# Kernel optimization log

Measured on AMD Instinct MI355X. Metric: run time of the kernel, lower is better.

## Reference

```python
import jax, jax.numpy as jnp
import numpy as np

N, E = 20000, 320000
IN_DIM = OUT_DIM = E_IN = E_OUT = 128
BN_EPS = 1e-5

def _lrelu(x):
    return jnp.where(x >= 0, x, 0.1 * x)

def setup_inputs() -> dict:
    key = jax.random.key(0)
    ks = jax.random.split(key, 12)
    def w(k, shape):
        return jax.random.normal(k, shape, jnp.float32) * (shape[0] ** -0.5)
    return {
        "h": jax.random.normal(ks[0], (N, IN_DIM), jnp.float32),
        "edge_w": jax.random.normal(ks[1], (E, E_IN), jnp.float32),
        "W_node": w(ks[2], (IN_DIM, OUT_DIM)),
        "W_eedge": w(ks[3], (E_IN, E_IN)),
        "W_esf": w(ks[4], (E_IN, 1)),
        "W_fuse": w(ks[5], (2 * OUT_DIM + E_IN, OUT_DIM)),
        "b_fuse": jnp.zeros((OUT_DIM,), jnp.float32),
        "W_attn": w(ks[6], (OUT_DIM, 1)),
        "W_conc": w(ks[7], (2 * OUT_DIM + E_IN, OUT_DIM)),
        "b_conc": jnp.zeros((OUT_DIM,), jnp.float32),
        "bn_gamma": jnp.ones((E_IN,), jnp.float32),
        "bn_beta": jnp.zeros((E_IN,), jnp.float32),
        "W_aggre": w(ks[8], (2 * OUT_DIM + 2 * E_IN, E_OUT)),
        "src": jax.random.randint(ks[9], (E,), 0, N),
        "dst": jax.random.randint(ks[10], (E,), 0, N),
    }

def reference(h, edge_w, W_node, W_eedge, W_esf, W_fuse, b_fuse, W_attn,
              W_conc, b_conc, bn_gamma, bn_beta, W_aggre, src, dst):
    # eval mode: dropout = identity, BatchNorm uses running stats (mean 0, var 1)
    hn = h @ W_node                       # embed_node -> ndata['h'] = ndata['oh']
    # self_attention: ow = embed_edge(w); w = edge_sf_atten(lrelu(ow)) * ow
    ow = edge_w @ W_eedge                 # [E, e_in]
    w1 = (_lrelu(ow) @ W_esf) * ow        # [E, e_in]
    # inter_attention
    hs, hd = hn[src], hn[dst]             # [E, out]
    sat = jnp.concatenate([hs, hd, w1], axis=-1)          # [E, 2*out+e_in]
    inw = _lrelu(sat @ W_fuse + b_fuse)                   # [E, out]
    a = inw @ W_attn                                      # [E, 1]
    w2 = a * w1                                           # edata['w']
    # reduce_func2: segment softmax over incoming edges (grouped by dst)
    s = a[:, 0]
    m = jax.ops.segment_max(s, dst, num_segments=N)
    e = jnp.exp(s - m[dst])
    denom = jax.ops.segment_sum(e, dst, num_segments=N)
    alpha = (e / denom[dst])[:, None]                     # [E, 1]
    t = jnp.concatenate([hs, w2], axis=-1)                # [E, out+e_in]
    h_agg = jax.ops.segment_sum(alpha * t, dst, num_segments=N)  # [N, out+e_in]
    h_new = jnp.concatenate([h_agg, hn], axis=-1) @ W_conc + b_conc
    # DGL only updates nodes that received messages; zero-indegree keep embed_node(h)
    indeg = jax.ops.segment_sum(jnp.ones((E,), jnp.float32), dst, num_segments=N)
    h_out = jnp.where(indeg[:, None] > 0, h_new, hn)      # [N, out]
    # edge_calc: BN(w2) then aggre_embed_edge(cat(src_h, dst_h, bn_w, ow))
    w_bn = (w2 / jnp.sqrt(jnp.float32(1.0) + BN_EPS)) * bn_gamma + bn_beta
    z = jnp.concatenate([h_out[src], h_out[dst], w_bn, ow], axis=-1)
    w_out = z @ W_aggre                                   # [E, e_out]
    return h_out, w_out, sat
```

## Files before the change

kernel.cpp:

```cpp
#include <hip/hip_runtime.h>
#include <hip/hip_bf16.h>

#define TB 256
#define TBM 512
#define BM 64
#define BK 32
#define BN 128
#define ASTR 68
#define MAXD 160

static constexpr int NN = 20000;
static constexpr int NE = 320000;

static constexpr long long OFF_HN   = 0;
static constexpr long long OFF_OW   = 2560000;
static constexpr long long OFF_S    = 43520000;
static constexpr long long OFF_DEN  = 43840000;
static constexpr long long OFF_CUR  = 43860000;
static constexpr long long OFF_HAGG = 43880000;
static constexpr long long OFF_WT   = 49000000;
static constexpr long long WS_FLOATS = 49140000;

static constexpr int U_E = 0;
static constexpr int U_F = 32768;
static constexpr int U_A = 131072;

static constexpr long long OUT_HOUT = 0;
static constexpr long long OUT_WOUT = 2560000;
static constexpr long long OUT_SAT  = 43520000;

typedef __attribute__((ext_vector_type(8))) short s8v;
typedef __attribute__((ext_vector_type(4))) float f32x4;
typedef __attribute__((ext_vector_type(8))) unsigned short u16x8;
typedef __attribute__((ext_vector_type(4))) unsigned short u16x4;

#define MFMA16(a,b,c) __builtin_amdgcn_mfma_f32_16x16x32_bf16(a,b,c,0,0,0)

__device__ __forceinline__ float lrelu(float x){ return x >= 0.f ? x : 0.1f*x; }

__device__ __forceinline__ void gl16(const void* g, void* l){
    __builtin_amdgcn_global_load_lds(
        (const __attribute__((address_space(1))) void*)g,
        (__attribute__((address_space(3))) void*)l, 16, 0, 0);
}

__device__ __forceinline__ void split1(float f, unsigned short& hi, unsigned short& lo){
    __hip_bfloat16 h = __float2bfloat16(f);
    float hf = __bfloat162float(h);
    __hip_bfloat16 l = __float2bfloat16(f - hf);
    hi = __builtin_bit_cast(unsigned short, h);
    lo = __builtin_bit_cast(unsigned short, l);
}
__device__ __forceinline__ void split8(float4 a, float4 b, s8v& hi, s8v& lo){
    float v[8] = {a.x,a.y,a.z,a.w,b.x,b.y,b.z,b.w};
#pragma unroll
    for (int j = 0; j < 8; ++j){
        unsigned short hs, ls;
        split1(v[j], hs, ls);
        hi[j] = (short)hs; lo[j] = (short)ls;
    }
}
__device__ __forceinline__ float bfpair(unsigned short h, unsigned short l){
    return __uint_as_float(((unsigned)h)<<16) + __uint_as_float(((unsigned)l)<<16);
}

__device__ __forceinline__ int lds_a(int row, int g){
    return row*32 + ((g ^ (row & 3)) << 3);
}

__device__ __forceinline__ void store_At(float (*Ast)[ASTR], int k4, int r, float4 v){
    Ast[k4+0][r] = v.x; Ast[k4+1][r] = v.y; Ast[k4+2][r] = v.z; Ast[k4+3][r] = v.w;
}
__device__ __forceinline__ void mm_chunk(const float (*Ast)[ASTR], const float (*Bs)[BN],
                                         int r0, int c0, float acc[4][8]){
#pragma unroll 4
    for (int k = 0; k < BK; ++k){
        const float4 av = *(const float4*)&Ast[k][r0];
        const float4 b0 = *(const float4*)&Bs[k][c0];
        const float4 b1 = *(const float4*)&Bs[k][64 + c0];
        const float a0=av.x, a1=av.y, a2=av.z, a3=av.w;
        const float b[8] = {b0.x,b0.y,b0.z,b0.w,b1.x,b1.y,b1.z,b1.w};
#pragma unroll
        for (int j = 0; j < 8; ++j){
            acc[0][j] = fmaf(a0, b[j], acc[0][j]);
            acc[1][j] = fmaf(a1, b[j], acc[1][j]);
            acc[2][j] = fmaf(a2, b[j], acc[2][j]);
            acc[3][j] = fmaf(a3, b[j], acc[3][j]);
        }
    }
}
__device__ __forceinline__ void load_B(const float* __restrict__ W, int kc,
                                       float (*Bs)[BN], int tid){
#pragma unroll
    for (int p = 0; p < 4; ++p){
        int idx = p*TB + tid;
        int row = idx >> 5;
        int c4  = (idx & 31) << 2;
        *(float4*)&Bs[row][c4] = *(const float4*)&W[(size_t)(kc+row)*BN + c4];
    }
}

__device__ __forceinline__ float blockMax(float v, float* sh4){
#pragma unroll
    for (int m = 32; m; m >>= 1) v = fmaxf(v, __shfl_xor(v, m));
    if ((threadIdx.x & 63) == 0) sh4[threadIdx.x >> 6] = v;
    __syncthreads();
    float r = fmaxf(fmaxf(sh4[0], sh4[1]), fmaxf(sh4[2], sh4[3]));
    __syncthreads();
    return r;
}
__device__ __forceinline__ float blockSum(float v, float* sh4){
#pragma unroll
    for (int m = 32; m; m >>= 1) v += __shfl_xor(v, m);
    if ((threadIdx.x & 63) == 0) sh4[threadIdx.x >> 6] = v;
    __syncthreads();
    float r = sh4[0] + sh4[1] + sh4[2] + sh4[3];
    __syncthreads();
    return r;
}

__global__ __launch_bounds__(TB) void k_prep(const float* __restrict__ We,
                                             const float* __restrict__ Wf,
                                             const float* __restrict__ Wa,
                                             unsigned short* __restrict__ wt,
                                             int* __restrict__ cur){
    int id = blockIdx.x*TB + threadIdx.x;
    if (id < NN) cur[id] = 0;
    unsigned short hs, ls;
    if (id < 16384){
        int n = id >> 7, k = id & 127;
        split1(We[(size_t)k*128 + n], hs, ls);
        wt[U_E + id] = hs; wt[U_E + 16384 + id] = ls;
    } else if (id < 65536){
        int local = id - 16384;
        int n = local / 384, k = local - n*384;
        split1(Wf[(size_t)k*128 + n], hs, ls);
        wt[U_F + local] = hs; wt[U_F + 49152 + local] = ls;
    } else if (id < 131072){
        int local = id - 65536;
        int n = local >> 9, k = local & 511;
        split1(Wa[(size_t)k*128 + n], hs, ls);
        wt[U_A + local] = hs; wt[U_A + 65536 + local] = ls;
    }
}

__global__ __launch_bounds__(TB) void kB_count(const int* __restrict__ dst,
                                               int* __restrict__ cur){
    int e = blockIdx.x*TB + threadIdx.x;
    atomicAdd(&cur[dst[e]], 1);
}
__global__ __launch_bounds__(TB) void kC_scan(int* __restrict__ cur,
                                              int* __restrict__ offs){
    __shared__ int part[TB];
    __shared__ int spre[TB];
    const int tid = threadIdx.x;
    const int CH = (NN + TB - 1) / TB;
    const int base = tid * CH;
    int sum = 0;
    for (int i = 0; i < CH; ++i){ int idx = base + i; if (idx < NN) sum += cur[idx]; }
    part[tid] = sum;
    __syncthreads();
    if (tid == 0){ int r = 0; for (int i = 0; i < TB; ++i){ spre[i] = r; r += part[i]; } }
    __syncthreads();
    int run = spre[tid];
    for (int i = 0; i < CH; ++i){
        int idx = base + i;
        if (idx < NN){ int c = cur[idx]; offs[idx] = run; cur[idx] = run; run += c; }
    }
}
__global__ __launch_bounds__(TB) void kD_scatter(const int* __restrict__ dst,
                                                 int* __restrict__ cur,
                                                 int* __restrict__ eidx){
    int e = blockIdx.x*TB + threadIdx.x;
    int p = atomicAdd(&cur[dst[e]], 1);
    eidx[p] = e;
}

__global__ __launch_bounds__(TB) void k1_hn(const float* __restrict__ h,
                                            const float* __restrict__ Wn,
                                            unsigned short* __restrict__ hnH,
                                            unsigned short* __restrict__ hnL){
    __shared__ float Ast[BK][ASTR];
    __shared__ float Bs[BK][BN];
    const int tid = threadIdx.x;
    const int rbase = blockIdx.x * BM;
    const int tc = tid & 15, tr = tid >> 4;
    const int r0 = tr*4, c0 = tc*4;
    float acc[4][8] = {};
    for (int kc = 0; kc < 128; kc += BK){
        __syncthreads();
        {
            int lr = tid >> 3, k4 = (tid & 7) << 2;
#pragma unroll
            for (int p = 0; p < 2; ++p){
                int r = p*32 + lr;
                int rr = rbase + r; if (rr >= NN) rr = NN-1;
                float4 v = *(const float4*)&h[(size_t)rr*128 + kc + k4];
                store_At(Ast, k4, r, v);
            }
        }
        load_B(Wn, kc, Bs, tid);
        __syncthreads();
        mm_chunk(Ast, Bs, r0, c0, acc);
    }
#pragma unroll
    for (int i = 0; i < 4; ++i){
        int rr = rbase + r0 + i;
        if (rr < NN){
            u16x4 h0, l0, h1, l1;
#pragma unroll
            for (int j = 0; j < 4; ++j){
                unsigned short hs, ls;
                split1(acc[i][j], hs, ls);   h0[j] = hs; l0[j] = ls;
                split1(acc[i][4+j], hs, ls); h1[j] = hs; l1[j] = ls;
            }
            *(u16x4*)&hnH[(size_t)rr*128 + c0] = h0;
            *(u16x4*)&hnL[(size_t)rr*128 + c0] = l0;
            *(u16x4*)&hnH[(size_t)rr*128 + 64 + c0] = h1;
            *(u16x4*)&hnL[(size_t)rr*128 + 64 + c0] = l1;
        }
    }
}


__global__ __launch_bounds__(TBM) void k2_mfma(const float* __restrict__ ew,
                                               const unsigned short* __restrict__ wtH,
                                               const unsigned short* __restrict__ wtL,
                                               const float* __restrict__ Wesf,
                                               unsigned short* __restrict__ owH,
                                               unsigned short* __restrict__ owL,
                                               float* __restrict__ sat){
    __shared__ __align__(16) unsigned short Ah[2][4096], Al[2][4096], Bh[2][4096], Bl[2][4096];
    __shared__ float sEsf[128];
    const int tid = threadIdx.x;
    const long long rbase = (long long)blockIdx.x * 128;
    const int lane = tid & 63, w = tid >> 6;
    const int ls = lane & 15, lg = lane >> 4;
    const int srow = tid >> 2, sg = tid & 3;
    const int gsw = sg ^ (srow & 3);
    const int aslot = srow*32 + (gsw << 3);
    if (tid < 128) sEsf[tid] = Wesf[tid];
    f32x4 acc[8] = {};
    auto stage = [&](int nb, int t){
        const int kc = t*32;
        gl16(&wtH[srow*128 + kc + gsw*8], &Bh[nb][w*512]);
        gl16(&wtL[srow*128 + kc + gsw*8], &Bl[nb][w*512]);
        const float* p = &ew[(rbase + srow)*128 + kc + sg*8];
        float4 v0 = *(const float4*)p, v1 = *(const float4*)(p+4);
        s8v hi, lo; split8(v0, v1, hi, lo);
        *(s8v*)&Ah[nb][aslot] = hi; *(s8v*)&Al[nb][aslot] = lo;
    };
    stage(0, 0);
    __syncthreads();
    int cur = 0;
    for (int t = 0; t < 4; ++t){
        if (t+1 < 4) stage(cur^1, t+1);
        s8v ah = *(const s8v*)&Ah[cur][lds_a(w*16 + ls, lg)];
        s8v al = *(const s8v*)&Al[cur][lds_a(w*16 + ls, lg)];
#pragma unroll
        for (int ct = 0; ct < 8; ++ct){
            int c = ct*16 + ls;
            s8v bh = *(const s8v*)&Bh[cur][lds_a(c,lg)];
            s8v bl = *(const s8v*)&Bl[cur][lds_a(c,lg)];
            acc[ct] = MFMA16(ah, bh, acc[ct]);
            acc[ct] = MFMA16(ah, bl, acc[ct]);
            acc[ct] = MFMA16(al, bh, acc[ct]);
        }
        __syncthreads();
        cur ^= 1;
    }
#pragma unroll
    for (int reg = 0; reg < 4; ++reg){
        float p = 0.f;
#pragma unroll
        for (int ct = 0; ct < 8; ++ct)
            p += lrelu(acc[ct][reg]) * sEsf[ct*16 + ls];
#pragma unroll
        for (int m = 1; m < 16; m <<= 1) p += __shfl_xor(p, m);
        long long orow = rbase + w*16 + lg*4 + reg;
#pragma unroll
        for (int ct = 0; ct < 8; ++ct){
            float o = acc[ct][reg];
            int col = ct*16 + ls;
            sat[orow*384 + 256 + col] = p * o;
            unsigned short hs_, ls_; split1(o, hs_, ls_);
            owH[orow*128 + col] = hs_;
            owL[orow*128 + col] = ls_;
        }
    }
}

__global__ __launch_bounds__(TBM) void k3_mfma(const unsigned short* __restrict__ hnH,
                                               const unsigned short* __restrict__ hnL,
                                               const unsigned short* __restrict__ wtH,
                                               const unsigned short* __restrict__ wtL,
                                               const float* __restrict__ bf,
                                               const float* __restrict__ Wattn,
                                               const int* __restrict__ src,
                                               const int* __restrict__ dst,
                                               float* __restrict__ sat,
                                               float* __restrict__ w2,
                                               float* __restrict__ s_ws){
    __shared__ __align__(16) unsigned short Ah[2][4096], Al[2][4096], Bh[2][4096], Bl[2][4096];
    __shared__ float sBf[128], sAtt[128];
    __shared__ int sSrc[128], sDst[128];
    const int tid = threadIdx.x;
    const long long rbase = (long long)blockIdx.x * 128;
    const int lane = tid & 63, w = tid >> 6;
    const int ls = lane & 15, lg = lane >> 4;
    const int srow = tid >> 2, sg = tid & 3;
    const int gsw = sg ^ (srow & 3);
    const int aslot = srow*32 + (gsw << 3);
    if (tid < 128){
        sBf[tid] = bf[tid]; sAtt[tid] = Wattn[tid];
        sSrc[tid] = src[rbase + tid]; sDst[tid] = dst[rbase + tid];
    }
    __syncthreads();
    f32x4 acc[8] = {};
    auto stage = [&](int nb, int t){
        const int kc = t*32;
        gl16(&wtH[srow*384 + kc + gsw*8], &Bh[nb][w*512]);
        gl16(&wtL[srow*384 + kc + gsw*8], &Bl[nb][w*512]);
        long long e = rbase + srow;
        if (kc < 256){
            int node = (kc < 128) ? sSrc[srow] : sDst[srow];
            int col0 = kc & 127;
            gl16(&hnH[(size_t)node*128 + col0 + gsw*8], &Ah[nb][w*512]);
            gl16(&hnL[(size_t)node*128 + col0 + gsw*8], &Al[nb][w*512]);
            u16x8 hv = *(const u16x8*)&hnH[(size_t)node*128 + col0 + sg*8];
            u16x8 lv = *(const u16x8*)&hnL[(size_t)node*128 + col0 + sg*8];
            float f[8];
#pragma unroll
            for (int j = 0; j < 8; ++j)
                f[j] = __uint_as_float(((unsigned)hv[j])<<16)
                     + __uint_as_float(((unsigned)lv[j])<<16);
            float4 v0 = {f[0],f[1],f[2],f[3]}, v1 = {f[4],f[5],f[6],f[7]};
            *(float4*)&sat[e*384 + kc + sg*8] = v0;
            *(float4*)&sat[e*384 + kc + sg*8 + 4] = v1;
        } else {
            const float* p = &sat[e*384 + kc + sg*8];
            float4 v0 = *(const float4*)p, v1 = *(const float4*)(p+4);
            s8v hi, lo; split8(v0, v1, hi, lo);
            *(s8v*)&Ah[nb][aslot] = hi; *(s8v*)&Al[nb][aslot] = lo;
        }
    };
    stage(0, 0);
    __syncthreads();
    int cur = 0;
    for (int t = 0; t < 12; ++t){
        if (t+1 < 12) stage(cur^1, t+1);
        s8v ah = *(const s8v*)&Ah[cur][lds_a(w*16 + ls, lg)];
        s8v al = *(const s8v*)&Al[cur][lds_a(w*16 + ls, lg)];
#pragma unroll
        for (int ct = 0; ct < 8; ++ct){
            int c = ct*16 + ls;
            s8v bh = *(const s8v*)&Bh[cur][lds_a(c,lg)];
            s8v bl = *(const s8v*)&Bl[cur][lds_a(c,lg)];
            acc[ct] = MFMA16(ah, bh, acc[ct]);
            acc[ct] = MFMA16(ah, bl, acc[ct]);
            acc[ct] = MFMA16(al, bh, acc[ct]);
        }
        __syncthreads();
        cur ^= 1;
    }
#pragma unroll
    for (int reg = 0; reg < 4; ++reg){
        float p = 0.f;
#pragma unroll
        for (int ct = 0; ct < 8; ++ct){
            int col = ct*16 + ls;
            p += lrelu(acc[ct][reg] + sBf[col]) * sAtt[col];
        }
#pragma unroll
        for (int m = 1; m < 16; m <<= 1) p += __shfl_xor(p, m);
        long long orow = rbase + w*16 + lg*4 + reg;
        if (ls == 0) s_ws[orow] = p;
#pragma unroll
        for (int ct = 0; ct < 8; ++ct){
            int col = ct*16 + ls;
            float w1v = sat[orow*384 + 256 + col];
            w2[orow*128 + col] = p * w1v;
        }
    }
}

__global__ __launch_bounds__(TB) void k5_agg(const float* __restrict__ s,
                                             const unsigned short* __restrict__ hnH,
                                             const unsigned short* __restrict__ hnL,
                                             const float* __restrict__ w2,
                                             const int* __restrict__ src,
                                             const int* __restrict__ eidx,
                                             const int* __restrict__ offs,
                                             const int* __restrict__ cur,
                                             float* __restrict__ hagg,
                                             float* __restrict__ den){
    __shared__ int   sE[MAXD];
    __shared__ int   sSrc[MAXD];
    __shared__ float sA[MAXD];
    __shared__ float sh4[4];
    const int n = blockIdx.x, tid = threadIdx.x;
    const int start = offs[n];
    const int deg = cur[n] - start;
    for (int i = tid; i < deg && i < MAXD; i += TB) sE[i] = eidx[start+i];
    __syncthreads();
    if (tid == 0 && deg > 1){
        int dd = deg < MAXD ? deg : MAXD;
        for (int i = 1; i < dd; ++i){
            int key = sE[i], j = i-1;
            while (j >= 0 && sE[j] > key){ sE[j+1] = sE[j]; --j; }
            sE[j+1] = key;
        }
    }
    __syncthreads();
    float lm = -3.402823466e38f;
    for (int i = tid; i < deg; i += TB){
        int e = (i < MAXD) ? sE[i] : eidx[start+i];
        lm = fmaxf(lm, s[e]);
    }
    const float m = blockMax(lm, sh4);
    float lsum = 0.f;
    for (int i = tid; i < deg; i += TB){
        int e = (i < MAXD) ? sE[i] : eidx[start+i];
        lsum += expf(s[e] - m);
    }
    const float denom = blockSum(lsum, sh4);
    for (int i = tid; i < deg && i < MAXD; i += TB){
        int e = sE[i];
        sA[i] = expf(s[e] - m) / denom;
        sSrc[i] = src[e];
    }
    __syncthreads();
    float acc = 0.f;
    const bool lo = tid < 128;
    for (int i = 0; i < deg; ++i){
        int e, sI; float a;
        if (i < MAXD){ e = sE[i]; a = sA[i]; sI = sSrc[i]; }
        else { e = eidx[start+i]; a = expf(s[e]-m)/denom; sI = src[e]; }
        float v = lo ? bfpair(hnH[(size_t)sI*128 + tid], hnL[(size_t)sI*128 + tid])
                     : w2[(size_t)e*128 + (tid-128)];
        acc = fmaf(a, v, acc);
    }
    hagg[(size_t)n*256 + tid] = acc;
    if (tid == 0) den[n] = (deg > 0) ? denom : 0.f;
}

__global__ __launch_bounds__(TB) void k6_conc(const float* hagg,
                                              const unsigned short* __restrict__ hnH,
                                              const unsigned short* __restrict__ hnL,
                                              const float* __restrict__ Wc,
                                              const float* __restrict__ bc,
                                              const float* __restrict__ den,
                                              float* __restrict__ hout,
                                              unsigned short* houtHL){
    __shared__ float Ast[BK][ASTR];
    __shared__ float Bs[BK][BN];
    __shared__ float sBc[BN];
    const int tid = threadIdx.x;
    const int rbase = blockIdx.x * BM;
    const int tc = tid & 15, tr = tid >> 4;
    const int r0 = tr*4, c0 = tc*4;
    if (tid < BN) sBc[tid] = bc[tid];
    float acc[4][8] = {};
    for (int chunk = 0; chunk < 12; ++chunk){
        int kc = chunk * BK;
        __syncthreads();
        {
            int lr = tid >> 3, k4 = (tid & 7) << 2;
#pragma unroll
            for (int p = 0; p < 2; ++p){
                int r = p*32 + lr;
                int rr = rbase + r; if (rr >= NN) rr = NN-1;
                float4 v;
                if (chunk < 8) v = *(const float4*)&hagg[(size_t)rr*256 + kc + k4];
                else {
                    int cb = (kc - 256) + k4;
                    u16x4 hh = *(const u16x4*)&hnH[(size_t)rr*128 + cb];
                    u16x4 ll = *(const u16x4*)&hnL[(size_t)rr*128 + cb];
                    v.x = bfpair(hh[0], ll[0]); v.y = bfpair(hh[1], ll[1]);
                    v.z = bfpair(hh[2], ll[2]); v.w = bfpair(hh[3], ll[3]);
                }
                store_At(Ast, k4, r, v);
            }
        }
        load_B(Wc, kc, Bs, tid);
        __syncthreads();
        mm_chunk(Ast, Bs, r0, c0, acc);
    }
#pragma unroll
    for (int i = 0; i < 4; ++i){
        int rr = rbase + r0 + i;
        if (rr >= NN) continue;
        bool keep = den[rr] > 0.f;
        float o[8];
#pragma unroll
        for (int j = 0; j < 8; ++j){
            int col = (j < 4) ? (c0 + j) : (60 + c0 + j);
            float fb = bfpair(hnH[(size_t)rr*128 + col], hnL[(size_t)rr*128 + col]);
            o[j] = keep ? acc[i][j] + sBc[col] : fb;
        }
        float4 o0 = {o[0],o[1],o[2],o[3]}, o1 = {o[4],o[5],o[6],o[7]};
        *(float4*)&hout[(size_t)rr*128 + c0] = o0;
        *(float4*)&hout[(size_t)rr*128 + 64 + c0] = o1;
        u16x4 h0, l0, h1, l1;
#pragma unroll
        for (int j = 0; j < 4; ++j){
            unsigned short hs, ls2;
            split1(o[j], hs, ls2);   h0[j] = hs; l0[j] = ls2;
            split1(o[4+j], hs, ls2); h1[j] = hs; l1[j] = ls2;
        }
        *(u16x4*)&houtHL[(size_t)rr*512 + c0] = h0;
        *(u16x4*)&houtHL[(size_t)rr*512 + 128 + c0] = l0;
        *(u16x4*)&houtHL[(size_t)rr*512 + 64 + c0] = h1;
        *(u16x4*)&houtHL[(size_t)rr*512 + 128 + 64 + c0] = l1;
    }
}

__global__ __launch_bounds__(TBM) void k7_mfma(const unsigned short* __restrict__ houtHL,
                                               const unsigned short* __restrict__ owH,
                                               const unsigned short* __restrict__ owL,
                                               const float* __restrict__ gamma,
                                               const float* __restrict__ beta,
                                               const unsigned short* __restrict__ wtH,
                                               const unsigned short* __restrict__ wtL,
                                               const int* __restrict__ src,
                                               const int* __restrict__ dst,
                                               float* __restrict__ w2out){
    __shared__ __align__(16) unsigned short Ah[2][4096], Al[2][4096], Bh[2][4096], Bl[2][4096];
    __shared__ float sGam[128], sBet[128];
    __shared__ int sSrc[128], sDst[128];
    const int tid = threadIdx.x;
    const long long rbase = (long long)blockIdx.x * 128;
    const int lane = tid & 63, w = tid >> 6;
    const int ls = lane & 15, lg = lane >> 4;
    const int srow = tid >> 2, sg = tid & 3;
    const int gsw = sg ^ (srow & 3);
    const int aslot = srow*32 + (gsw << 3);
    const float ISR = 0.9999950000374997f;
    if (tid < 128){
        sGam[tid] = gamma[tid] * ISR; sBet[tid] = beta[tid];
        sSrc[tid] = src[rbase + tid]; sDst[tid] = dst[rbase + tid];
    }
    __syncthreads();
    f32x4 acc[8] = {};
    auto stage = [&](int nb, int t){
        const int kc = t*32;
        gl16(&wtH[srow*512 + kc + gsw*8], &Bh[nb][w*512]);
        gl16(&wtL[srow*512 + kc + gsw*8], &Bl[nb][w*512]);
        long long e = rbase + srow;
        if (kc < 256){
            int node = (kc < 128) ? sSrc[srow] : sDst[srow];
            int col0 = kc & 127;
            gl16(&houtHL[(size_t)node*512 + col0 + gsw*8], &Ah[nb][w*512]);
            gl16(&houtHL[(size_t)node*512 + 128 + col0 + gsw*8], &Al[nb][w*512]);
        } else if (kc < 384){
            int cb = (kc - 256) + sg*8;
            const float* p = &w2out[e*128 + cb];
            float4 v0 = *(const float4*)p, v1 = *(const float4*)(p+4);
            v0.x = fmaf(v0.x, sGam[cb+0], sBet[cb+0]);
            v0.y = fmaf(v0.y, sGam[cb+1], sBet[cb+1]);
            v0.z = fmaf(v0.z, sGam[cb+2], sBet[cb+2]);
            v0.w = fmaf(v0.w, sGam[cb+3], sBet[cb+3]);
            v1.x = fmaf(v1.x, sGam[cb+4], sBet[cb+4]);
            v1.y = fmaf(v1.y, sGam[cb+5], sBet[cb+5]);
            v1.z = fmaf(v1.z, sGam[cb+6], sBet[cb+6]);
            v1.w = fmaf(v1.w, sGam[cb+7], sBet[cb+7]);
            s8v hi, lo; split8(v0, v1, hi, lo);
            *(s8v*)&Ah[nb][aslot] = hi; *(s8v*)&Al[nb][aslot] = lo;
        } else {
            int col0 = kc - 384;
            gl16(&owH[e*128 + col0 + gsw*8], &Ah[nb][w*512]);
            gl16(&owL[e*128 + col0 + gsw*8], &Al[nb][w*512]);
        }
    };
    stage(0, 0);
    __syncthreads();
    int cur = 0;
    for (int t = 0; t < 16; ++t){
        if (t+1 < 16) stage(cur^1, t+1);
        s8v ah = *(const s8v*)&Ah[cur][lds_a(w*16 + ls, lg)];
        s8v al = *(const s8v*)&Al[cur][lds_a(w*16 + ls, lg)];
#pragma unroll
        for (int ct = 0; ct < 8; ++ct){
            int c = ct*16 + ls;
            s8v bh = *(const s8v*)&Bh[cur][lds_a(c,lg)];
            s8v bl = *(const s8v*)&Bl[cur][lds_a(c,lg)];
            acc[ct] = MFMA16(ah, bh, acc[ct]);
            acc[ct] = MFMA16(ah, bl, acc[ct]);
            acc[ct] = MFMA16(al, bh, acc[ct]);
        }
        __syncthreads();
        cur ^= 1;
    }
#pragma unroll
    for (int reg = 0; reg < 4; ++reg){
        long long orow = rbase + w*16 + lg*4 + reg;
#pragma unroll
        for (int ct = 0; ct < 8; ++ct)
            w2out[orow*128 + ct*16 + ls] = acc[ct][reg];
    }
}

extern "C" void kernel_launch(void* const* d_in, const int* in_sizes, int n_in,
                              void* d_out, int out_size, void* d_ws, size_t ws_size,
                              hipStream_t stream){
    (void)in_sizes; (void)n_in; (void)out_size;
    const float* h       = (const float*)d_in[0];
    const float* edge_w  = (const float*)d_in[1];
    const float* W_node  = (const float*)d_in[2];
    const float* W_eedge = (const float*)d_in[3];
    const float* W_esf   = (const float*)d_in[4];
    const float* W_fuse  = (const float*)d_in[5];
    const float* b_fuse  = (const float*)d_in[6];
    const float* W_attn  = (const float*)d_in[7];
    const float* W_conc  = (const float*)d_in[8];
    const float* b_conc  = (const float*)d_in[9];
    const float* gamma   = (const float*)d_in[10];
    const float* beta    = (const float*)d_in[11];
    const float* W_aggre = (const float*)d_in[12];
    const int*   src     = (const int*)d_in[13];
    const int*   dst     = (const int*)d_in[14];

    float* out    = (float*)d_out;
    float* o_hout = out + OUT_HOUT;
    float* o_wout = out + OUT_WOUT;
    float* o_sat  = out + OUT_SAT;

    if (ws_size < (size_t)WS_FLOATS * 4) return;
    float* ws     = (float*)d_ws;
    unsigned short* w_hnH = (unsigned short*)(ws + OFF_HN);
    unsigned short* w_hnL = w_hnH + (size_t)NN*128;
    unsigned short* w_owH = (unsigned short*)(ws + OFF_OW);
    unsigned short* w_owL = w_owH + (size_t)NE*128;
    float* w_s    = ws + OFF_S;
    float* w_den  = ws + OFF_DEN;
    int*   w_cur  = (int*)(ws + OFF_CUR);
    float* w_hagg = ws + OFF_HAGG;
    unsigned short* w_houtHL = (unsigned short*)w_hagg;
    unsigned short* w_wt = (unsigned short*)(ws + OFF_WT);

    int* w_eidx = (int*)o_hout;
    int* w_offs = w_eidx + NE;

    hipLaunchKernelGGL(k_prep,    dim3(131072/TB), dim3(TB), 0, stream,
                       W_eedge, W_fuse, W_aggre, w_wt, w_cur);
    hipLaunchKernelGGL(kB_count,  dim3(NE/TB), dim3(TB), 0, stream, dst, w_cur);
    hipLaunchKernelGGL(kC_scan,   dim3(1), dim3(TB), 0, stream, w_cur, w_offs);
    hipLaunchKernelGGL(kD_scatter,dim3(NE/TB), dim3(TB), 0, stream, dst, w_cur, w_eidx);
    hipLaunchKernelGGL(k1_hn,     dim3((NN+BM-1)/BM), dim3(TB), 0, stream, h, W_node,
                       w_hnH, w_hnL);
    hipLaunchKernelGGL(k2_mfma,   dim3(NE/128), dim3(TBM), 0, stream, edge_w,
                       w_wt + U_E, w_wt + U_E + 128*128, W_esf,
                       w_owH, w_owL, o_sat);
    hipLaunchKernelGGL(k3_mfma,   dim3(NE/128), dim3(TBM), 0, stream, w_hnH, w_hnL,
                       w_wt + U_F, w_wt + U_F + 128*384, b_fuse, W_attn,
                       src, dst, o_sat, o_wout, w_s);
    hipLaunchKernelGGL(k5_agg,    dim3(NN), dim3(TB), 0, stream, w_s, w_hnH, w_hnL, o_wout,
                       src, w_eidx, w_offs, w_cur, w_hagg, w_den);
    hipLaunchKernelGGL(k6_conc,   dim3((NN+BM-1)/BM), dim3(TB), 0, stream, w_hagg,
                       w_hnH, w_hnL, W_conc, b_conc, w_den, o_hout, w_houtHL);
    hipLaunchKernelGGL(k7_mfma,   dim3(NE/128), dim3(TBM), 0, stream, w_houtHL,
                       w_owH, w_owL, gamma, beta,
                       w_wt + U_A, w_wt + U_A + 128*512,
                       src, dst, o_wout);
}
```

Before: 834.4 us.

## Pack hn hi/lo pairs, drop w2 materialization, use wave-per-node aggregation

k1_hn now also writes a packed array holding each bf16 hi/lo pair in one 32-bit word, kept in the w_out output buffer as scratch. k3, k5 and k6 read that packed array instead of two separate 16-bit arrays. k3 no longer writes the E×128 w2 tensor: k5 and k7 rebuild it from w1 (stored in sat) scaled by the per-edge attention score s. k5 runs one 64-lane wave per node, four nodes per block, and replaces the single-thread insertion sort and block-wide reductions with a parallel rank sort and wave shuffles. The aim is to cut global memory traffic and serialization, at the cost of an extra packed write in k1 and more strided reads of sat.

```diff
diff --git a/kernel.cpp b/kernel.cpp
--- a/kernel.cpp
+++ b/kernel.cpp
@@ -31,7 +31,6 @@
 
 typedef __attribute__((ext_vector_type(8))) short s8v;
 typedef __attribute__((ext_vector_type(4))) float f32x4;
-typedef __attribute__((ext_vector_type(8))) unsigned short u16x8;
 typedef __attribute__((ext_vector_type(4))) unsigned short u16x4;
 
 #define MFMA16(a,b,c) __builtin_amdgcn_mfma_f32_16x16x32_bf16(a,b,c,0,0,0)
@@ -60,8 +59,8 @@
         hi[j] = (short)hs; lo[j] = (short)ls;
     }
 }
-__device__ __forceinline__ float bfpair(unsigned short h, unsigned short l){
-    return __uint_as_float(((unsigned)h)<<16) + __uint_as_float(((unsigned)l)<<16);
+__device__ __forceinline__ float bfp(unsigned p){
+    return __uint_as_float(p & 0xffff0000u) + __uint_as_float(p << 16);
 }
 
 __device__ __forceinline__ int lds_a(int row, int g){
@@ -98,25 +97,6 @@
         int c4  = (idx & 31) << 2;
         *(float4*)&Bs[row][c4] = *(const float4*)&W[(size_t)(kc+row)*BN + c4];
     }
-}
-
-__device__ __forceinline__ float blockMax(float v, float* sh4){
-#pragma unroll
-    for (int m = 32; m; m >>= 1) v = fmaxf(v, __shfl_xor(v, m));
-    if ((threadIdx.x & 63) == 0) sh4[threadIdx.x >> 6] = v;
-    __syncthreads();
-    float r = fmaxf(fmaxf(sh4[0], sh4[1]), fmaxf(sh4[2], sh4[3]));
-    __syncthreads();
-    return r;
-}
-__device__ __forceinline__ float blockSum(float v, float* sh4){
-#pragma unroll
-    for (int m = 32; m; m >>= 1) v += __shfl_xor(v, m);
-    if ((threadIdx.x & 63) == 0) sh4[threadIdx.x >> 6] = v;
-    __syncthreads();
-    float r = sh4[0] + sh4[1] + sh4[2] + sh4[3];
-    __syncthreads();
-    return r;
 }
 
 __global__ __launch_bounds__(TB) void k_prep(const float* __restrict__ We,
@@ -179,7 +159,8 @@
 __global__ __launch_bounds__(TB) void k1_hn(const float* __restrict__ h,
                                             const float* __restrict__ Wn,
                                             unsigned short* __restrict__ hnH,
-                                            unsigned short* __restrict__ hnL){
+                                            unsigned short* __restrict__ hnL,
+                                            unsigned* __restrict__ hnP){
     __shared__ float Ast[BK][ASTR];
     __shared__ float Bs[BK][BN];
     const int tid = threadIdx.x;
@@ -208,16 +189,23 @@
         int rr = rbase + r0 + i;
         if (rr < NN){
             u16x4 h0, l0, h1, l1;
+            uint4 p0, p1;
 #pragma unroll
             for (int j = 0; j < 4; ++j){
                 unsigned short hs, ls;
-                split1(acc[i][j], hs, ls);   h0[j] = hs; l0[j] = ls;
-                split1(acc[i][4+j], hs, ls); h1[j] = hs; l1[j] = ls;
+                split1(acc[i][j], hs, ls);
+                h0[j] = hs; l0[j] = ls;
+                ((unsigned*)&p0)[j] = ((unsigned)hs << 16) | ls;
+                split1(acc[i][4+j], hs, ls);
+                h1[j] = hs; l1[j] = ls;
+                ((unsigned*)&p1)[j] = ((unsigned)hs << 16) | ls;
             }
             *(u16x4*)&hnH[(size_t)rr*128 + c0] = h0;
             *(u16x4*)&hnL[(size_t)rr*128 + c0] = l0;
             *(u16x4*)&hnH[(size_t)rr*128 + 64 + c0] = h1;
             *(u16x4*)&hnL[(size_t)rr*128 + 64 + c0] = l1;
+            *(uint4*)&hnP[(size_t)rr*128 + c0] = p0;
+            *(uint4*)&hnP[(size_t)rr*128 + 64 + c0] = p1;
         }
     }
 }
@@ -292,6 +280,7 @@
 
 __global__ __launch_bounds__(TBM) void k3_mfma(const unsigned short* __restrict__ hnH,
                                                const unsigned short* __restrict__ hnL,
+                                               const unsigned* __restrict__ hnP,
                                                const unsigned short* __restrict__ wtH,
                                                const unsigned short* __restrict__ wtL,
                                                const float* __restrict__ bf,
@@ -299,7 +288,6 @@
                                                const int* __restrict__ src,
                                                const int* __restrict__ dst,
                                                float* __restrict__ sat,
-                                               float* __restrict__ w2,
                                                float* __restrict__ s_ws){
     __shared__ __align__(16) unsigned short Ah[2][4096], Al[2][4096], Bh[2][4096], Bl[2][4096];
     __shared__ float sBf[128], sAtt[128];
@@ -327,14 +315,10 @@
             int col0 = kc & 127;
             gl16(&hnH[(size_t)node*128 + col0 + gsw*8], &Ah[nb][w*512]);
             gl16(&hnL[(size_t)node*128 + col0 + gsw*8], &Al[nb][w*512]);
-            u16x8 hv = *(const u16x8*)&hnH[(size_t)node*128 + col0 + sg*8];
-            u16x8 lv = *(const u16x8*)&hnL[(size_t)node*128 + col0 + sg*8];
-            float f[8];
-#pragma unroll
-            for (int j = 0; j < 8; ++j)
-                f[j] = __uint_as_float(((unsigned)hv[j])<<16)
-                     + __uint_as_float(((unsigned)lv[j])<<16);
-            float4 v0 = {f[0],f[1],f[2],f[3]}, v1 = {f[4],f[5],f[6],f[7]};
+            const unsigned* pp = &hnP[(size_t)node*128 + col0 + sg*8];
+            uint4 q0 = *(const uint4*)pp, q1 = *(const uint4*)(pp+4);
+            float4 v0 = {bfp(q0.x), bfp(q0.y), bfp(q0.z), bfp(q0.w)};
+            float4 v1 = {bfp(q1.x), bfp(q1.y), bfp(q1.z), bfp(q1.w)};
             *(float4*)&sat[e*384 + kc + sg*8] = v0;
             *(float4*)&sat[e*384 + kc + sg*8 + 4] = v1;
         } else {
@@ -373,80 +357,102 @@
         }
 #pragma unroll
         for (int m = 1; m < 16; m <<= 1) p += __shfl_xor(p, m);
-        long long orow = rbase + w*16 + lg*4 + reg;
-        if (ls == 0) s_ws[orow] = p;
-#pragma unroll
-        for (int ct = 0; ct < 8; ++ct){
-            int col = ct*16 + ls;
-            float w1v = sat[orow*384 + 256 + col];
-            w2[orow*128 + col] = p * w1v;
-        }
+        if (ls == 0) s_ws[rbase + w*16 + lg*4 + reg] = p;
     }
 }
 
 __global__ __launch_bounds__(TB) void k5_agg(const float* __restrict__ s,
-                                             const unsigned short* __restrict__ hnH,
-                                             const unsigned short* __restrict__ hnL,
-                                             const float* __restrict__ w2,
+                                             const unsigned* __restrict__ hnP,
+                                             const float* __restrict__ sat,
                                              const int* __restrict__ src,
                                              const int* __restrict__ eidx,
                                              const int* __restrict__ offs,
                                              const int* __restrict__ cur,
                                              float* __restrict__ hagg,
                                              float* __restrict__ den){
-    __shared__ int   sE[MAXD];
-    __shared__ int   sSrc[MAXD];
-    __shared__ float sA[MAXD];
-    __shared__ float sh4[4];
-    const int n = blockIdx.x, tid = threadIdx.x;
+    __shared__ int   sEu[4][MAXD];
+    __shared__ int   sEs[4][MAXD];
+    __shared__ float sAl[4][MAXD];
+    __shared__ float sWc[4][MAXD];
+    const int wv = threadIdx.x >> 6, lane = threadIdx.x & 63;
+    const int n = blockIdx.x*4 + wv;
+    int* Eu = sEu[wv]; int* Es = sEs[wv];
+    float* Al = sAl[wv]; float* Wc = sWc[wv];
     const int start = offs[n];
     const int deg = cur[n] - start;
-    for (int i = tid; i < deg && i < MAXD; i += TB) sE[i] = eidx[start+i];
-    __syncthreads();
-    if (tid == 0 && deg > 1){
-        int dd = deg < MAXD ? deg : MAXD;
-        for (int i = 1; i < dd; ++i){
-            int key = sE[i], j = i-1;
-            while (j >= 0 && sE[j] > key){ sE[j+1] = sE[j]; --j; }
-            sE[j+1] = key;
-        }
+    const int dc = deg < MAXD ? deg : MAXD;
+    for (int i = lane; i < dc; i += 64) Eu[i] = eidx[start+i];
+    __syncthreads();
+    for (int i = lane; i < dc; i += 64){
+        int my = Eu[i], r = 0;
+        for (int j = 0; j < dc; ++j) r += (Eu[j] < my);
+        Es[r] = my;
     }
     __syncthreads();
     float lm = -3.402823466e38f;
-    for (int i = tid; i < deg; i += TB){
-        int e = (i < MAXD) ? sE[i] : eidx[start+i];
-        lm = fmaxf(lm, s[e]);
-    }
-    const float m = blockMax(lm, sh4);
+    for (int i = lane; i < dc; i += 64){
+        int e = Es[i];
+        float sv = s[e];
+        Wc[i] = sv;
+        Eu[i] = src[e];
+        lm = fmaxf(lm, sv);
+    }
+    for (int i = MAXD + lane; i < deg; i += 64) lm = fmaxf(lm, s[eidx[start+i]]);
+#pragma unroll
+    for (int m2 = 32; m2; m2 >>= 1) lm = fmaxf(lm, __shfl_xor(lm, m2));
+    const float m = lm;
     float lsum = 0.f;
-    for (int i = tid; i < deg; i += TB){
-        int e = (i < MAXD) ? sE[i] : eidx[start+i];
-        lsum += expf(s[e] - m);
-    }
-    const float denom = blockSum(lsum, sh4);
-    for (int i = tid; i < deg && i < MAXD; i += TB){
-        int e = sE[i];
-        sA[i] = expf(s[e] - m) / denom;
-        sSrc[i] = src[e];
-    }
-    __syncthreads();
-    float acc = 0.f;
-    const bool lo = tid < 128;
-    for (int i = 0; i < deg; ++i){
-        int e, sI; float a;
-        if (i < MAXD){ e = sE[i]; a = sA[i]; sI = sSrc[i]; }
-        else { e = eidx[start+i]; a = expf(s[e]-m)/denom; sI = src[e]; }
-        float v = lo ? bfpair(hnH[(size_t)sI*128 + tid], hnL[(size_t)sI*128 + tid])
-                     : w2[(size_t)e*128 + (tid-128)];
-        acc = fmaf(a, v, acc);
-    }
-    hagg[(size_t)n*256 + tid] = acc;
-    if (tid == 0) den[n] = (deg > 0) ? denom : 0.f;
+    for (int i = lane; i < dc; i += 64){
+        float ev = expf(Wc[i] - m);
+        Al[i] = ev;
+        lsum += ev;
+    }
+    for (int i = MAXD + lane; i < deg; i += 64) lsum += expf(s[eidx[start+i]] - m);
+#pragma unroll
+    for (int m2 = 32; m2; m2 >>= 1) lsum += __shfl_xor(lsum, m2);
+    const float denom = lsum;
+    const float inv = (deg > 0) ? 1.f/denom : 0.f;
+    for (int i = lane; i < dc; i += 64){
+        float al = Al[i] * inv;
+        Al[i] = al;
+        Wc[i] = al * Wc[i];
+    }
+    __syncthreads();
+    float a0=0.f, a1=0.f, a2=0.f, a3=0.f;
+    for (int i = 0; i < dc; ++i){
+        int sI = Eu[i];
+        size_t e = (size_t)Es[i];
+        float al = Al[i], wc = Wc[i];
+        unsigned p0 = hnP[(size_t)sI*128 + lane];
+        unsigned p1 = hnP[(size_t)sI*128 + 64 + lane];
+        float w0 = sat[e*384 + 256 + lane];
+        float w1v = sat[e*384 + 256 + 64 + lane];
+        a0 = fmaf(al, bfp(p0), a0);
+        a1 = fmaf(al, bfp(p1), a1);
+        a2 = fmaf(wc, w0, a2);
+        a3 = fmaf(wc, w1v, a3);
+    }
+    for (int i = MAXD; i < deg; ++i){
+        int e = eidx[start+i];
+        float sv = s[e];
+        float al = expf(sv - m) * inv;
+        float wc = al * sv;
+        int sI = src[e];
+        a0 = fmaf(al, bfp(hnP[(size_t)sI*128 + lane]), a0);
+        a1 = fmaf(al, bfp(hnP[(size_t)sI*128 + 64 + lane]), a1);
+        a2 = fmaf(wc, sat[(size_t)e*384 + 256 + lane], a2);
+        a3 = fmaf(wc, sat[(size_t)e*384 + 256 + 64 + lane], a3);
+    }
+    const size_t b = (size_t)n*256;
+    hagg[b + lane] = a0;
+    hagg[b + 64 + lane] = a1;
+    hagg[b + 128 + lane] = a2;
+    hagg[b + 192 + lane] = a3;
+    if (lane == 0) den[n] = (deg > 0) ? denom : 0.f;
 }
 
 __global__ __launch_bounds__(TB) void k6_conc(const float* hagg,
-                                              const unsigned short* __restrict__ hnH,
-                                              const unsigned short* __restrict__ hnL,
+                                              const unsigned* __restrict__ hnP,
                                               const float* __restrict__ Wc,
                                               const float* __restrict__ bc,
                                               const float* __restrict__ den,
@@ -474,10 +480,8 @@
                 if (chunk < 8) v = *(const float4*)&hagg[(size_t)rr*256 + kc + k4];
                 else {
                     int cb = (kc - 256) + k4;
-                    u16x4 hh = *(const u16x4*)&hnH[(size_t)rr*128 + cb];
-                    u16x4 ll = *(const u16x4*)&hnL[(size_t)rr*128 + cb];
-                    v.x = bfpair(hh[0], ll[0]); v.y = bfpair(hh[1], ll[1]);
-                    v.z = bfpair(hh[2], ll[2]); v.w = bfpair(hh[3], ll[3]);
+                    uint4 q = *(const uint4*)&hnP[(size_t)rr*128 + cb];
+                    v.x = bfp(q.x); v.y = bfp(q.y); v.z = bfp(q.z); v.w = bfp(q.w);
                 }
                 store_At(Ast, k4, r, v);
             }
@@ -495,7 +499,7 @@
 #pragma unroll
         for (int j = 0; j < 8; ++j){
             int col = (j < 4) ? (c0 + j) : (60 + c0 + j);
-            float fb = bfpair(hnH[(size_t)rr*128 + col], hnL[(size_t)rr*128 + col]);
+            float fb = bfp(hnP[(size_t)rr*128 + col]);
             o[j] = keep ? acc[i][j] + sBc[col] : fb;
         }
         float4 o0 = {o[0],o[1],o[2],o[3]}, o1 = {o[4],o[5],o[6],o[7]};
@@ -518,6 +522,8 @@
 __global__ __launch_bounds__(TBM) void k7_mfma(const unsigned short* __restrict__ houtHL,
                                                const unsigned short* __restrict__ owH,
                                                const unsigned short* __restrict__ owL,
+                                               const float* __restrict__ sarr,
+                                               const float* __restrict__ sat,
                                                const float* __restrict__ gamma,
                                                const float* __restrict__ beta,
                                                const unsigned short* __restrict__ wtH,
@@ -526,7 +532,7 @@
                                                const int* __restrict__ dst,
                                                float* __restrict__ w2out){
     __shared__ __align__(16) unsigned short Ah[2][4096], Al[2][4096], Bh[2][4096], Bl[2][4096];
-    __shared__ float sGam[128], sBet[128];
+    __shared__ float sGam[128], sBet[128], sS[128];
     __shared__ int sSrc[128], sDst[128];
     const int tid = threadIdx.x;
     const long long rbase = (long long)blockIdx.x * 128;
@@ -539,6 +545,7 @@
     if (tid < 128){
         sGam[tid] = gamma[tid] * ISR; sBet[tid] = beta[tid];
         sSrc[tid] = src[rbase + tid]; sDst[tid] = dst[rbase + tid];
+        sS[tid] = sarr[rbase + tid];
     }
     __syncthreads();
     f32x4 acc[8] = {};
@@ -554,16 +561,17 @@
             gl16(&houtHL[(size_t)node*512 + 128 + col0 + gsw*8], &Al[nb][w*512]);
         } else if (kc < 384){
             int cb = (kc - 256) + sg*8;
-            const float* p = &w2out[e*128 + cb];
+            float se = sS[srow];
+            const float* p = &sat[e*384 + 256 + cb];
             float4 v0 = *(const float4*)p, v1 = *(const float4*)(p+4);
-            v0.x = fmaf(v0.x, sGam[cb+0], sBet[cb+0]);
-            v0.y = fmaf(v0.y, sGam[cb+1], sBet[cb+1]);
-            v0.z = fmaf(v0.z, sGam[cb+2], sBet[cb+2]);
-            v0.w = fmaf(v0.w, sGam[cb+3], sBet[cb+3]);
-            v1.x = fmaf(v1.x, sGam[cb+4], sBet[cb+4]);
-            v1.y = fmaf(v1.y, sGam[cb+5], sBet[cb+5]);
-            v1.z = fmaf(v1.z, sGam[cb+6], sBet[cb+6]);
-            v1.w = fmaf(v1.w, sGam[cb+7], sBet[cb+7]);
+            v0.x = fmaf(v0.x*se, sGam[cb+0], sBet[cb+0]);
+            v0.y = fmaf(v0.y*se, sGam[cb+1], sBet[cb+1]);
+            v0.z = fmaf(v0.z*se, sGam[cb+2], sBet[cb+2]);
+            v0.w = fmaf(v0.w*se, sGam[cb+3], sBet[cb+3]);
+            v1.x = fmaf(v1.x*se, sGam[cb+4], sBet[cb+4]);
+            v1.y = fmaf(v1.y*se, sGam[cb+5], sBet[cb+5]);
+            v1.z = fmaf(v1.z*se, sGam[cb+6], sBet[cb+6]);
+            v1.w = fmaf(v1.w*se, sGam[cb+7], sBet[cb+7]);
             s8v hi, lo; split8(v0, v1, hi, lo);
             *(s8v*)&Ah[nb][aslot] = hi; *(s8v*)&Al[nb][aslot] = lo;
         } else {
@@ -638,6 +646,7 @@
     unsigned short* w_houtHL = (unsigned short*)w_hagg;
     unsigned short* w_wt = (unsigned short*)(ws + OFF_WT);
 
+    unsigned* w_hnP = (unsigned*)o_wout;
     int* w_eidx = (int*)o_hout;
     int* w_offs = w_eidx + NE;
 
@@ -647,19 +656,19 @@
     hipLaunchKernelGGL(kC_scan,   dim3(1), dim3(TB), 0, stream, w_cur, w_offs);
     hipLaunchKernelGGL(kD_scatter,dim3(NE/TB), dim3(TB), 0, stream, dst, w_cur, w_eidx);
     hipLaunchKernelGGL(k1_hn,     dim3((NN+BM-1)/BM), dim3(TB), 0, stream, h, W_node,
-                       w_hnH, w_hnL);
+                       w_hnH, w_hnL, w_hnP);
     hipLaunchKernelGGL(k2_mfma,   dim3(NE/128), dim3(TBM), 0, stream, edge_w,
                        w_wt + U_E, w_wt + U_E + 128*128, W_esf,
                        w_owH, w_owL, o_sat);
-    hipLaunchKernelGGL(k3_mfma,   dim3(NE/128), dim3(TBM), 0, stream, w_hnH, w_hnL,
+    hipLaunchKernelGGL(k3_mfma,   dim3(NE/128), dim3(TBM), 0, stream, w_hnH, w_hnL, w_hnP,
                        w_wt + U_F, w_wt + U_F + 128*384, b_fuse, W_attn,
-                       src, dst, o_sat, o_wout, w_s);
-    hipLaunchKernelGGL(k5_agg,    dim3(NN), dim3(TB), 0, stream, w_s, w_hnH, w_hnL, o_wout,
+                       src, dst, o_sat, w_s);
+    hipLaunchKernelGGL(k5_agg,    dim3(NN/4), dim3(TB), 0, stream, w_s, w_hnP, o_sat,
                        src, w_eidx, w_offs, w_cur, w_hagg, w_den);
     hipLaunchKernelGGL(k6_conc,   dim3((NN+BM-1)/BM), dim3(TB), 0, stream, w_hagg,
-                       w_hnH, w_hnL, W_conc, b_conc, w_den, o_hout, w_houtHL);
+                       w_hnP, W_conc, b_conc, w_den, o_hout, w_houtHL);
     hipLaunchKernelGGL(k7_mfma,   dim3(NE/128), dim3(TBM), 0, stream, w_houtHL,
-                       w_owH, w_owL, gamma, beta,
+                       w_owH, w_owL, w_s, o_sat, gamma, beta,
                        w_wt + U_A, w_wt + U_A + 128*512,
                        src, dst, o_wout);
 }
```

Result: faster. 711.5 us (-14.7%).
